# Kernel optimization log

Hardware: AMD Instinct MI355X
Metric: run time of the kernel (lower is better)

The kernel has to match this reference:

```python
import jax, jax.numpy as jnp
import numpy as np

N = 100000   # nodes
E = 1600000  # edges (before self-loops)
HIDDEN = 256
BN_EPS = 1e-5


def setup_inputs() -> dict:
    key = jax.random.key(0)
    ks = jax.random.split(key, 16)
    def lin(k, i, o):
        return jax.random.normal(k, (i, o), jnp.float32) / np.float32(np.sqrt(i))
    inp = {
        "x": jax.random.normal(ks[0], (N, 21), jnp.float32),
        "edge_index": jax.random.randint(ks[1], (2, E), 0, N),
        # GCNConv weights (stored [in, out]) + biases
        "W1": lin(ks[2], 21, HIDDEN), "b1": jnp.zeros((HIDDEN,), jnp.float32),
        "W2": lin(ks[3], HIDDEN, 112), "b2": jnp.zeros((112,), jnp.float32),
        # dense MLP
        "lin2_w": lin(ks[4], 112, 256), "lin2_b": jnp.zeros((256,), jnp.float32),
        "lin3_w": lin(ks[5], 256, 100), "lin3_b": jnp.zeros((100,), jnp.float32),
        "lin4_w": lin(ks[6], 100, 1),   "lin4_b": jnp.zeros((1,), jnp.float32),
        # batchnorm affine params
        "g1": jnp.ones((112,), jnp.float32), "be1": jnp.zeros((112,), jnp.float32),
        "g2": jnp.ones((256,), jnp.float32), "be2": jnp.zeros((256,), jnp.float32),
        "g3": jnp.ones((100,), jnp.float32), "be3": jnp.zeros((100,), jnp.float32),
    }
    return inp


def _gcn_conv(x, W, b, src, dst, n):
    # PyG GCNConv: h = xW; out_i = sum_j norm_ij * h_j (+ bias), sym-normalized w/ self-loops
    h = x @ W                                              # [N, C]
    deg = jax.ops.segment_sum(jnp.ones(src.shape, h.dtype), dst, num_segments=n)
    dinv = jnp.where(deg > 0, jax.lax.rsqrt(deg), 0.0)
    norm = dinv[src] * dinv[dst]                            # [E']
    out = jax.ops.segment_sum(h[src] * norm[:, None], dst, num_segments=n)
    return out + b


def _bn(x, g, b):
    # train-mode batchnorm: biased batch variance
    m = jnp.mean(x, axis=0)
    v = jnp.mean(jnp.square(x - m), axis=0)
    return (x - m) * jax.lax.rsqrt(v + BN_EPS) * g + b


def reference(x, edge_index, W1, b1, W2, b2, lin2_w, lin2_b, lin3_w, lin3_b,
              lin4_w, lin4_b, g1, be1, g2, be2, g3, be3):
    n = x.shape[0]
    loops = jnp.arange(n, dtype=edge_index.dtype)
    src = jnp.concatenate([edge_index[0], loops])
    dst = jnp.concatenate([edge_index[1], loops])
    h = jax.nn.relu(_gcn_conv(x, W1, b1, src, dst, n))
    h = _gcn_conv(h, W2, b2, src, dst, n)
    h = jax.nn.relu(_bn(h, g1, be1))
    # dropout: identity (eval / deterministic)
    h = jax.nn.relu(_bn(h @ lin2_w + lin2_b, g2, be2))
    h = jax.nn.relu(_bn(h @ lin3_w + lin3_b, g3, be3))
    return h @ lin4_w + lin4_b
```

## Files before the change

kernel.cpp:

```cpp
#include <hip/hip_runtime.h>

#define N_NODES 100000
#define N_EDGES 1600000

typedef _Float16 f16x8 __attribute__((ext_vector_type(8)));
typedef _Float16 f16x4 __attribute__((ext_vector_type(4)));
typedef float fx4 __attribute__((ext_vector_type(4)));

#define NREP 16
#define NBUCK 196
#define CHUNK 8192
#define BCAP 12288

__global__ __launch_bounds__(256) void k_bin(const int* __restrict__ ei,
                                             unsigned* __restrict__ binned,
                                             int* __restrict__ gcount) {
  __shared__ unsigned pr[CHUNK];
  __shared__ unsigned srt[CHUNK];
  __shared__ unsigned char bk[CHUNK];
  __shared__ int hist[256], scanb[256], offs[256], bs[256], gb[256];
  const int t = threadIdx.x;
  const int e0 = blockIdx.x * CHUNK;
  const int n = min(CHUNK, N_EDGES - e0);
  hist[t] = 0;
  __syncthreads();
  for (int i = t; i < n; i += 256) {
    int src = ei[e0 + i], dst = ei[N_EDGES + e0 + i];
    int b = dst >> 9;
    pr[i] = ((unsigned)src << 9) | (unsigned)(dst & 511);
    bk[i] = (unsigned char)b;
    atomicAdd(&hist[b], 1);
  }
  __syncthreads();
  int v = hist[t];
  scanb[t] = v;
  __syncthreads();
  for (int off = 1; off < 256; off <<= 1) {
    int a = (t >= off) ? scanb[t - off] : 0;
    __syncthreads();
    scanb[t] += a;
    __syncthreads();
  }
  offs[t] = scanb[t] - v;
  bs[t] = scanb[t] - v;
  __syncthreads();
  for (int i = t; i < n; i += 256) {
    int b = bk[i];
    int p = atomicAdd(&offs[b], 1);
    srt[p] = pr[i];
  }
  if (t < NBUCK && v > 0) gb[t] = atomicAdd(&gcount[t], v);
  __syncthreads();
  int wave = t >> 6, lane = t & 63;
  for (int b = wave; b < NBUCK; b += 4) {
    int c = hist[b];
    if (c == 0) continue;
    int ls = bs[b], base = gb[b];
    unsigned* dstp = binned + (size_t)b * BCAP + base;
    for (int i = lane; i < c; i += 64) dstp[i] = srt[ls + i];
  }
}

__global__ void k_bscan(const int* __restrict__ gcount, int* __restrict__ gbase) {
  __shared__ int s[256];
  int t = threadIdx.x;
  int v = (t < NBUCK) ? gcount[t] : 0;
  s[t] = v;
  __syncthreads();
  for (int off = 1; off < 256; off <<= 1) {
    int a = (t >= off) ? s[t - off] : 0;
    __syncthreads();
    s[t] += a;
    __syncthreads();
  }
  if (t < NBUCK) gbase[t] = s[t] - v;
}

__global__ __launch_bounds__(256) void k_csr(const unsigned* __restrict__ binned,
                                             const int* __restrict__ gcount,
                                             const int* __restrict__ gbase,
                                             int* __restrict__ rowoff,
                                             int* __restrict__ cnt,
                                             float* __restrict__ dinv,
                                             int* __restrict__ csr) {
  __shared__ int hist[512], offs[512], ps[256];
  __shared__ unsigned srt[BCAP];
  const int b = blockIdx.x, t = threadIdx.x;
  const int n = min(gcount[b], BCAP);
  const int gb0 = gbase[b];
  const unsigned* bp = binned + (size_t)b * BCAP;
  hist[t] = 0;
  hist[t + 256] = 0;
  __syncthreads();
  for (int i = t; i < n; i += 256) atomicAdd(&hist[bp[i] & 511], 1);
  __syncthreads();
  int e0v = hist[2 * t], e1v = hist[2 * t + 1];
  ps[t] = e0v + e1v;
  __syncthreads();
  for (int off = 1; off < 256; off <<= 1) {
    int a = (t >= off) ? ps[t - off] : 0;
    __syncthreads();
    ps[t] += a;
    __syncthreads();
  }
  int excl = ps[t] - (e0v + e1v);
  offs[2 * t] = excl;
  offs[2 * t + 1] = excl + e0v;
  __syncthreads();
#pragma unroll
  for (int u = 0; u < 2; ++u) {
    int j = 2 * t + u;
    int nd = (b << 9) + j;
    if (nd < N_NODES) {
      int c = hist[j];
      cnt[nd] = c;
      dinv[nd] = rsqrtf((float)(c + 1));
      rowoff[nd] = gb0 + offs[j];
    }
  }
  __syncthreads();
  for (int i = t; i < n; i += 256) {
    unsigned p = bp[i];
    int d = p & 511;
    int pos = atomicAdd(&offs[d], 1);
    srt[pos] = p >> 9;
  }
  __syncthreads();
  for (int i = t; i < n; i += 256) csr[gb0 + i] = (int)srt[i];
}

__global__ void k_xpad(const float* __restrict__ x, const float* __restrict__ dinv,
                       _Float16* __restrict__ xs) {
  int idx = blockIdx.x * 256 + threadIdx.x;
  if (idx >= N_NODES * 24) return;
  int r = idx / 24, c = idx - r * 24;
  xs[idx] = (_Float16)((c < 21) ? x[r * 21 + c] * dinv[r] : 0.f);
}

__global__ __launch_bounds__(256) void k_aggx(
    const f16x8* __restrict__ xs3, const float* __restrict__ dinv,
    const int* __restrict__ rowoff, const int* __restrict__ cnt,
    const int* __restrict__ csr, float* __restrict__ aggx) {
  int lane = threadIdx.x & 63, wave = threadIdx.x >> 6;
  int j = lane / 3, c = lane - j * 3;
  if (j >= 21) return;
  int i = blockIdx.x * 84 + wave * 21 + j;
  if (i >= N_NODES) return;
  float di = dinv[i];
  int start = rowoff[i], len = cnt[i];
  f16x8 u = xs3[i * 3 + c];
  float a0[8], a1[8], a2[8], a3[8];
#pragma unroll
  for (int t = 0; t < 8; ++t) { a0[t] = (float)u[t]; a1[t] = a2[t] = a3[t] = 0.f; }
  int e = 0;
  for (; e + 3 < len; e += 4) {
    int s0 = csr[start + e], s1 = csr[start + e + 1];
    int s2 = csr[start + e + 2], s3 = csr[start + e + 3];
    f16x8 u0 = xs3[s0 * 3 + c];
    f16x8 u1 = xs3[s1 * 3 + c];
    f16x8 u2 = xs3[s2 * 3 + c];
    f16x8 u3 = xs3[s3 * 3 + c];
#pragma unroll
    for (int t = 0; t < 8; ++t) {
      a0[t] += (float)u0[t]; a1[t] += (float)u1[t];
      a2[t] += (float)u2[t]; a3[t] += (float)u3[t];
    }
  }
  for (; e < len; ++e) {
    int s0 = csr[start + e];
    f16x8 u0 = xs3[s0 * 3 + c];
#pragma unroll
    for (int t = 0; t < 8; ++t) a0[t] += (float)u0[t];
  }
  float4 r0, r1;
  r0.x = di * (a0[0] + a1[0] + a2[0] + a3[0]);
  r0.y = di * (a0[1] + a1[1] + a2[1] + a3[1]);
  r0.z = di * (a0[2] + a1[2] + a2[2] + a3[2]);
  r0.w = di * (a0[3] + a1[3] + a2[3] + a3[3]);
  r1.x = di * (a0[4] + a1[4] + a2[4] + a3[4]);
  r1.y = di * (a0[5] + a1[5] + a2[5] + a3[5]);
  r1.z = di * (a0[6] + a1[6] + a2[6] + a3[6]);
  r1.w = di * (a0[7] + a1[7] + a2[7] + a3[7]);
  *(float4*)(aggx + (size_t)i * 24 + c * 8) = r0;
  *(float4*)(aggx + (size_t)i * 24 + c * 8 + 4) = r1;
}

__global__ __launch_bounds__(256) void k_gemm1(const float4* __restrict__ aggx4,
                                               const float* __restrict__ W1,
                                               const float* __restrict__ b1,
                                               _Float16* __restrict__ h1) {
  __shared__ float As[32][24];
  int t = threadIdx.x;
  int base = blockIdx.x * 32;
  for (int idx = t; idx < 32 * 6; idx += 256) {
    int m = idx / 6, q = idx - m * 6;
    *(float4*)(&As[m][q * 4]) = aggx4[(base + m) * 6 + q];
  }
  float w[21];
#pragma unroll
  for (int k = 0; k < 21; ++k) w[k] = W1[k * 256 + t];
  float bias = b1[t];
  __syncthreads();
  for (int m = 0; m < 32; ++m) {
    float acc = bias;
#pragma unroll
    for (int k = 0; k < 21; ++k) acc = fmaf(As[m][k], w[k], acc);
    h1[(size_t)(base + m) * 256 + t] = (_Float16)fmaxf(acc, 0.f);
  }
}

template <int K, int KPAD, int NOUT, int NR>
__global__ void k_wcvt(const float* __restrict__ W, _Float16* __restrict__ Wh) {
  int idx = blockIdx.x * 256 + threadIdx.x;
  if (idx >= NR * KPAD) return;
  int n = idx / KPAD, k = idx % KPAD;
  float v = (n < NOUT && k < K) ? W[k * NOUT + n] : 0.f;
  Wh[idx] = (_Float16)v;
}

template <int K, int KPAD, int NT, int MT, int WR, int WC, int MINW,
          bool BN, bool STATS, bool F16OUT, bool SPLIT>
__global__ __launch_bounds__(256, MINW) void k_mgemm(
    const _Float16* __restrict__ A16, const _Float16* __restrict__ Wt,
    const float* __restrict__ bias, const float* __restrict__ bn_a,
    const float* __restrict__ bn_c, const float* __restrict__ rowscale,
    void* __restrict__ Cv, void* __restrict__ Cv2, int NOUTr,
    float* __restrict__ sums, float* __restrict__ sqs) {
  constexpr int BM = WR * MT * 16;
  constexpr int NR = WC * NT * 16;
  constexpr int BKP = 40;
  constexpr int NC = KPAD / 32;
  constexpr int AIT = BM * 4 / 256;
  constexpr int ABYTES = BM * BKP * 2;
  constexpr int BBYTES = NR * BKP * 2;
  __shared__ __align__(16) char smem[ABYTES + BBYTES];
  _Float16* Ah = (_Float16*)smem;
  _Float16* Bh = (_Float16*)(smem + ABYTES);
  float* C = (float*)Cv;
  _Float16* C16 = (_Float16*)Cv;
  _Float16* C16b = (_Float16*)Cv2;

  const int tid = threadIdx.x;
  const int lane = tid & 63, wave = tid >> 6;
  const int wr = wave % WR, wc = wave / WR;
  const int quad = lane >> 4, ln = lane & 15;
  const int rowbase = blockIdx.x * BM;

  fx4 acc[MT][NT];
#pragma unroll
  for (int mt = 0; mt < MT; ++mt)
#pragma unroll
    for (int j = 0; j < NT; ++j) acc[mt][j] = (fx4){0.f, 0.f, 0.f, 0.f};

  f16x8 pf16[AIT];

  auto loadA = [&](int kc) {
#pragma unroll
    for (int it = 0; it < AIT; ++it) {
      int idx = tid + it * 256;
      int m = idx >> 2, q = idx & 3;
      int gi = rowbase + m;
      int k = kc * 32 + q * 8;
      bool ok = (gi < N_NODES) && (k < K);
      f16x8 z;
#pragma unroll
      for (int t = 0; t < 8; ++t) z[t] = (_Float16)0;
      pf16[it] = ok ? *(const f16x8*)(A16 + (size_t)gi * K + k) : z;
    }
  };

  auto writeA = [&](int kc) {
#pragma unroll
    for (int it = 0; it < AIT; ++it) {
      int idx = tid + it * 256;
      int m = idx >> 2, q = idx & 3;
      int k = kc * 32 + q * 8;
      float vv[8];
#pragma unroll
      for (int t = 0; t < 8; ++t) vv[t] = (float)pf16[it][t];
      if constexpr (BN) {
        if (k < K) {
          float4 a0 = *(const float4*)(bn_a + k);
          float4 a1 = *(const float4*)(bn_a + k + 4);
          float4 c0 = *(const float4*)(bn_c + k);
          float4 c1 = *(const float4*)(bn_c + k + 4);
          float av[8] = {a0.x, a0.y, a0.z, a0.w, a1.x, a1.y, a1.z, a1.w};
          float cv[8] = {c0.x, c0.y, c0.z, c0.w, c1.x, c1.y, c1.z, c1.w};
#pragma unroll
          for (int t = 0; t < 8; ++t) vv[t] = fmaxf(fmaf(vv[t], av[t], cv[t]), 0.f);
        }
      }
      f16x8 hv;
#pragma unroll
      for (int t = 0; t < 8; ++t) hv[t] = (_Float16)vv[t];
      *(f16x8*)(Ah + m * BKP + q * 8) = hv;
    }
  };

  loadA(0);
  for (int kc = 0; kc < NC; ++kc) {
    __syncthreads();
    writeA(kc);
    for (int idx = tid; idx < NR * 4; idx += 256) {
      int n = idx >> 2, p = idx & 3;
      *(f16x8*)(Bh + n * BKP + p * 8) =
          *(const f16x8*)(Wt + n * KPAD + kc * 32 + p * 8);
    }
    __syncthreads();
    if (kc + 1 < NC) loadA(kc + 1);
    f16x8 nf[MT];
#pragma unroll
    for (int mt = 0; mt < MT; ++mt) {
      int r = (wr * MT + mt) * 16 + ln;
      nf[mt] = *(const f16x8*)(Ah + r * BKP + quad * 8);
    }
#pragma unroll
    for (int j = 0; j < NT; ++j) {
      int n = (wc * NT + j) * 16 + ln;
      f16x8 wh = *(const f16x8*)(Bh + n * BKP + quad * 8);
#pragma unroll
      for (int mt = 0; mt < MT; ++mt)
        acc[mt][j] = __builtin_amdgcn_mfma_f32_16x16x32_f16(wh, nf[mt], acc[mt][j], 0, 0, 0);
    }
  }

  float* s_s = (float*)smem;
  float* s_q = s_s + NR;
  __syncthreads();
  if constexpr (STATS) {
    for (int c = tid; c < 2 * NR; c += 256) s_s[c] = 0.f;
    __syncthreads();
  }
  float rs[MT];
#pragma unroll
  for (int mt = 0; mt < MT; ++mt) {
    int nd = rowbase + (wr * MT + mt) * 16 + ln;
    rs[mt] = (rowscale != nullptr && nd < N_NODES) ? rowscale[nd] : 1.f;
  }
#pragma unroll
  for (int j = 0; j < NT; ++j) {
    int ch0 = (wc * NT + j) * 16 + quad * 4;
    bool cv = ch0 < NOUTr;
    float4 b4 = make_float4(0.f, 0.f, 0.f, 0.f);
    if (cv && bias != nullptr) b4 = *(const float4*)(bias + ch0);
    float sc[4] = {0.f, 0.f, 0.f, 0.f}, sq[4] = {0.f, 0.f, 0.f, 0.f};
#pragma unroll
    for (int mt = 0; mt < MT; ++mt) {
      int nd = rowbase + (wr * MT + mt) * 16 + ln;
      if (nd < N_NODES && cv) {
        float v0 = (acc[mt][j][0] + b4.x) * rs[mt];
        float v1 = (acc[mt][j][1] + b4.y) * rs[mt];
        float v2 = (acc[mt][j][2] + b4.z) * rs[mt];
        float v3 = (acc[mt][j][3] + b4.w) * rs[mt];
        if constexpr (F16OUT) {
          f16x4 o = {(_Float16)v0, (_Float16)v1, (_Float16)v2, (_Float16)v3};
          if constexpr (SPLIT) {
            _Float16* dp = (ch0 < 56)
                ? C16 + (size_t)nd * 64 + ch0
                : C16b + (size_t)nd * 64 + (ch0 - 56);
            *(f16x4*)dp = o;
          } else {
            *(f16x4*)(C16 + (size_t)nd * NOUTr + ch0) = o;
          }
        } else {
          float4 o = make_float4(v0, v1, v2, v3);
          *(float4*)(C + (size_t)nd * NOUTr + ch0) = o;
        }
        if constexpr (STATS) {
          sc[0] += v0; sq[0] = fmaf(v0, v0, sq[0]);
          sc[1] += v1; sq[1] = fmaf(v1, v1, sq[1]);
          sc[2] += v2; sq[2] = fmaf(v2, v2, sq[2]);
          sc[3] += v3; sq[3] = fmaf(v3, v3, sq[3]);
        }
      }
    }
    if constexpr (STATS) {
      if (cv) {
#pragma unroll
        for (int r = 0; r < 4; ++r) {
          float s = sc[r], q = sq[r];
          s += __shfl_xor(s, 1); q += __shfl_xor(q, 1);
          s += __shfl_xor(s, 2); q += __shfl_xor(q, 2);
          s += __shfl_xor(s, 4); q += __shfl_xor(q, 4);
          s += __shfl_xor(s, 8); q += __shfl_xor(q, 8);
          if (ln == 0) {
            atomicAdd(&s_s[ch0 + r], s);
            atomicAdd(&s_q[ch0 + r], q);
          }
        }
      }
    }
  }
  if constexpr (STATS) {
    __syncthreads();
    int rep = (blockIdx.x & (NREP - 1));
    for (int c = tid; c < NR; c += 256) {
      if (c < NOUTr) {
        atomicAdd(&sums[rep * NOUTr + c], s_s[c]);
        atomicAdd(&sqs[rep * NOUTr + c], s_q[c]);
      }
    }
  }
}

template <int K, int KPAD, int NT, int MT, int MINW,
          bool BN, bool STATS, bool F16OUT>
__global__ __launch_bounds__(256, MINW) void k_mgemm2(
    const _Float16* __restrict__ A16, const _Float16* __restrict__ Wt,
    const float* __restrict__ bias, const float* __restrict__ bn_a,
    const float* __restrict__ bn_c, const float* __restrict__ rowscale,
    void* __restrict__ Cv, int NOUTr, float* __restrict__ sums,
    float* __restrict__ sqs) {
  constexpr int WR = 4;
  constexpr int BM = WR * MT * 16;
  constexpr int NR = NT * 16;
  constexpr int KPS = KPAD + 8;
  constexpr int NC = KPAD / 32;
  __shared__ __align__(16) _Float16 Bh[NR * KPS];

  const int tid = threadIdx.x;
  const int lane = tid & 63, wave = tid >> 6;
  const int quad = lane >> 4, ln = lane & 15;
  const int rowbase = blockIdx.x * BM;
  const int chbase = blockIdx.y * NR;

  for (int idx = tid; idx < NR * (KPAD / 8); idx += 256) {
    int n = idx / (KPAD / 8), p = idx % (KPAD / 8);
    *(f16x8*)(Bh + n * KPS + p * 8) =
        *(const f16x8*)(Wt + (size_t)(chbase + n) * KPAD + p * 8);
  }
  __syncthreads();

  fx4 acc[MT][NT];
#pragma unroll
  for (int mt = 0; mt < MT; ++mt)
#pragma unroll
    for (int j = 0; j < NT; ++j) acc[mt][j] = (fx4){0.f, 0.f, 0.f, 0.f};

  for (int kc = 0; kc < NC; ++kc) {
    const int k0 = kc * 32 + quad * 8;
    f16x8 af[MT];
#pragma unroll
    for (int mt = 0; mt < MT; ++mt) {
      int gi = rowbase + (wave * MT + mt) * 16 + ln;
      bool ok = (gi < N_NODES) && (k0 < K);
      f16x8 z;
#pragma unroll
      for (int t = 0; t < 8; ++t) z[t] = (_Float16)0;
      af[mt] = ok ? *(const f16x8*)(A16 + (size_t)gi * K + k0) : z;
    }
    if constexpr (BN) {
      if (k0 < K) {
        float4 ba0 = *(const float4*)(bn_a + k0);
        float4 ba1 = *(const float4*)(bn_a + k0 + 4);
        float4 bc0 = *(const float4*)(bn_c + k0);
        float4 bc1 = *(const float4*)(bn_c + k0 + 4);
        float av[8] = {ba0.x, ba0.y, ba0.z, ba0.w, ba1.x, ba1.y, ba1.z, ba1.w};
        float cv[8] = {bc0.x, bc0.y, bc0.z, bc0.w, bc1.x, bc1.y, bc1.z, bc1.w};
#pragma unroll
        for (int mt = 0; mt < MT; ++mt)
#pragma unroll
          for (int t = 0; t < 8; ++t)
            af[mt][t] = (_Float16)fmaxf(fmaf((float)af[mt][t], av[t], cv[t]), 0.f);
      }
    }
#pragma unroll
    for (int j = 0; j < NT; ++j) {
      f16x8 wh = *(const f16x8*)(Bh + (j * 16 + ln) * KPS + kc * 32 + quad * 8);
#pragma unroll
      for (int mt = 0; mt < MT; ++mt)
        acc[mt][j] = __builtin_amdgcn_mfma_f32_16x16x32_f16(wh, af[mt], acc[mt][j], 0, 0, 0);
    }
  }

  float* s_s = (float*)Bh;
  float* s_q = s_s + NR;
  __syncthreads();
  if constexpr (STATS) {
    for (int c = tid; c < 2 * NR; c += 256) s_s[c] = 0.f;
    __syncthreads();
  }
  float rs[MT];
#pragma unroll
  for (int mt = 0; mt < MT; ++mt) {
    int nd = rowbase + (wave * MT + mt) * 16 + ln;
    rs[mt] = (rowscale != nullptr && nd < N_NODES) ? rowscale[nd] : 1.f;
  }
  float* C = (float*)Cv;
  _Float16* C16 = (_Float16*)Cv;
#pragma unroll
  for (int j = 0; j < NT; ++j) {
    int lch = j * 16 + quad * 4;
    int ch0 = chbase + lch;
    bool cv = ch0 < NOUTr;
    float4 b4 = make_float4(0.f, 0.f, 0.f, 0.f);
    if (cv && bias != nullptr) b4 = *(const float4*)(bias + ch0);
    float sc[4] = {0.f, 0.f, 0.f, 0.f}, sq[4] = {0.f, 0.f, 0.f, 0.f};
#pragma unroll
    for (int mt = 0; mt < MT; ++mt) {
      int nd = rowbase + (wave * MT + mt) * 16 + ln;
      if (nd < N_NODES && cv) {
        float v0 = (acc[mt][j][0] + b4.x) * rs[mt];
        float v1 = (acc[mt][j][1] + b4.y) * rs[mt];
        float v2 = (acc[mt][j][2] + b4.z) * rs[mt];
        float v3 = (acc[mt][j][3] + b4.w) * rs[mt];
        if constexpr (F16OUT) {
          f16x4 o = {(_Float16)v0, (_Float16)v1, (_Float16)v2, (_Float16)v3};
          *(f16x4*)(C16 + (size_t)nd * NOUTr + ch0) = o;
        } else {
          float4 o = make_float4(v0, v1, v2, v3);
          *(float4*)(C + (size_t)nd * NOUTr + ch0) = o;
        }
        if constexpr (STATS) {
          sc[0] += v0; sq[0] = fmaf(v0, v0, sq[0]);
          sc[1] += v1; sq[1] = fmaf(v1, v1, sq[1]);
          sc[2] += v2; sq[2] = fmaf(v2, v2, sq[2]);
          sc[3] += v3; sq[3] = fmaf(v3, v3, sq[3]);
        }
      }
    }
    if constexpr (STATS) {
      if (cv) {
#pragma unroll
        for (int r = 0; r < 4; ++r) {
          float s = sc[r], q = sq[r];
          s += __shfl_xor(s, 1); q += __shfl_xor(q, 1);
          s += __shfl_xor(s, 2); q += __shfl_xor(q, 2);
          s += __shfl_xor(s, 4); q += __shfl_xor(q, 4);
          s += __shfl_xor(s, 8); q += __shfl_xor(q, 8);
          if (ln == 0) {
            atomicAdd(&s_s[lch + r], s);
            atomicAdd(&s_q[lch + r], q);
          }
        }
      }
    }
  }
  if constexpr (STATS) {
    __syncthreads();
    int rep = (blockIdx.x & (NREP - 1));
    for (int c = tid; c < NR; c += 256) {
      int gc = chbase + c;
      if (gc < NOUTr) {
        atomicAdd(&sums[rep * NOUTr + gc], s_s[c]);
        atomicAdd(&sqs[rep * NOUTr + gc], s_q[c]);
      }
    }
  }
}

__global__ __launch_bounds__(256) void k_agg2(
    const f16x8* __restrict__ t2x8, const float* __restrict__ dinv,
    const int* __restrict__ rowoff, const int* __restrict__ cnt,
    const int* __restrict__ csr, const float* __restrict__ b2,
    _Float16* __restrict__ g2, int off) {
  int lane = threadIdx.x & 63, wave = threadIdx.x >> 6;
  int j = lane >> 3, c = lane & 7;
  int i = blockIdx.x * 32 + wave * 8 + j;
  float di = dinv[i];
  int start = rowoff[i], len = cnt[i];
  f16x8 u = t2x8[i * 8 + c];
  float a0[8], a1[8], a2[8], a3[8];
#pragma unroll
  for (int t = 0; t < 8; ++t) { a0[t] = (float)u[t]; a1[t] = a2[t] = a3[t] = 0.f; }
  int e = 0;
  for (; e + 3 < len; e += 4) {
    int s0 = csr[start + e], s1 = csr[start + e + 1];
    int s2 = csr[start + e + 2], s3 = csr[start + e + 3];
    f16x8 u0 = t2x8[s0 * 8 + c];
    f16x8 u1 = t2x8[s1 * 8 + c];
    f16x8 u2 = t2x8[s2 * 8 + c];
    f16x8 u3 = t2x8[s3 * 8 + c];
#pragma unroll
    for (int t = 0; t < 8; ++t) {
      a0[t] += (float)u0[t]; a1[t] += (float)u1[t];
      a2[t] += (float)u2[t]; a3[t] += (float)u3[t];
    }
  }
  for (; e < len; ++e) {
    int s0 = csr[start + e];
    f16x8 u0 = t2x8[s0 * 8 + c];
#pragma unroll
    for (int t = 0; t < 8; ++t) a0[t] += (float)u0[t];
  }
  if (c < 7) {
    float4 blo = *(const float4*)(b2 + off + c * 8);
    float4 bhi = *(const float4*)(b2 + off + c * 8 + 4);
    float bb[8] = {blo.x, blo.y, blo.z, blo.w, bhi.x, bhi.y, bhi.z, bhi.w};
    f16x8 o;
#pragma unroll
    for (int t = 0; t < 8; ++t)
      o[t] = (_Float16)fmaf(di, a0[t] + a1[t] + a2[t] + a3[t], bb[t]);
    *(f16x8*)(g2 + (size_t)i * 112 + off + c * 8) = o;
  }
}

template <int C>
__global__ void k_colstats16(const _Float16* __restrict__ X, float* __restrict__ sums,
                             float* __restrict__ sqs) {
  int c = threadIdx.x;
  if (c >= C) return;
  int chunk = (N_NODES + gridDim.x - 1) / gridDim.x;
  int i0 = blockIdx.x * chunk;
  int i1 = min(N_NODES, i0 + chunk);
  float s = 0.f, q = 0.f;
  for (int i = i0; i < i1; ++i) {
    float v = (float)X[(size_t)i * C + c];
    s += v;
    q = fmaf(v, v, q);
  }
  int rep = (blockIdx.x & (NREP - 1));
  atomicAdd(&sums[rep * C + c], s);
  atomicAdd(&sqs[rep * C + c], q);
}

template <int C>
__global__ void k_bnfinal(const float* __restrict__ sums, const float* __restrict__ sqs,
                          const float* __restrict__ gamma, const float* __restrict__ beta,
                          float* __restrict__ bn_a, float* __restrict__ bn_c) {
  int c = threadIdx.x;
  if (c >= C) return;
  float s = 0.f, q = 0.f;
#pragma unroll
  for (int r = 0; r < NREP; ++r) {
    s += sums[r * C + c];
    q += sqs[r * C + c];
  }
  const float inv_n = 1.0f / (float)N_NODES;
  float mean = s * inv_n;
  float var = fmaxf(q * inv_n - mean * mean, 0.f);
  float rstd = 1.0f / sqrtf(var + 1e-5f);
  float a = gamma[c] * rstd;
  bn_a[c] = a;
  bn_c[c] = beta[c] - mean * a;
}

__global__ void k_final(const _Float16* __restrict__ h4, const float* __restrict__ bn_a,
                        const float* __restrict__ bn_c, const float* __restrict__ w4,
                        const float* __restrict__ b4, float* __restrict__ out) {
  int lane = threadIdx.x & 63;
  int i = blockIdx.x * 4 + (threadIdx.x >> 6);
  float acc = fmaxf(fmaf((float)h4[(size_t)i * 100 + lane], bn_a[lane], bn_c[lane]), 0.f) * w4[lane];
  if (lane < 36) {
    int k = lane + 64;
    acc += fmaxf(fmaf((float)h4[(size_t)i * 100 + k], bn_a[k], bn_c[k]), 0.f) * w4[k];
  }
#pragma unroll
  for (int off = 32; off >= 1; off >>= 1) acc += __shfl_down(acc, off);
  if (lane == 0) out[i] = acc + b4[0];
}

extern "C" void kernel_launch(void* const* d_in, const int* in_sizes, int n_in,
                              void* d_out, int out_size, void* d_ws, size_t ws_size,
                              hipStream_t stream) {
  const float* x   = (const float*)d_in[0];
  const int*   ei  = (const int*)d_in[1];
  const float* W1  = (const float*)d_in[2];
  const float* b1  = (const float*)d_in[3];
  const float* W2  = (const float*)d_in[4];
  const float* b2  = (const float*)d_in[5];
  const float* l2w = (const float*)d_in[6];
  const float* l2b = (const float*)d_in[7];
  const float* l3w = (const float*)d_in[8];
  const float* l3b = (const float*)d_in[9];
  const float* l4w = (const float*)d_in[10];
  const float* l4b = (const float*)d_in[11];
  const float* g1  = (const float*)d_in[12];
  const float* be1 = (const float*)d_in[13];
  const float* g2w = (const float*)d_in[14];
  const float* be2 = (const float*)d_in[15];
  const float* g3  = (const float*)d_in[16];
  const float* be3 = (const float*)d_in[17];
  float* out = (float*)d_out;

  char* base = (char*)d_ws;
  size_t off = 0;
  auto alloc = [&](size_t bytes) -> char* {
    char* p = base + off;
    off = (off + bytes + 255) & ~(size_t)255;
    return p;
  };
  int*   cnt    = (int*)alloc((size_t)N_NODES * 4);
  int*   rowoff = (int*)alloc((size_t)N_NODES * 4);
  float* dinv   = (float*)alloc((size_t)N_NODES * 4);
  int*   csr    = (int*)alloc((size_t)N_EDGES * 4);
  unsigned* binned = (unsigned*)alloc((size_t)NBUCK * BCAP * 4);
  int*   gcount = (int*)alloc(NBUCK * 4);
  int*   gbase  = (int*)alloc(NBUCK * 4);
  float* stats  = (float*)alloc((size_t)NREP * 960 * 4);
  float* bnco   = (float*)alloc(960 * 4);
  _Float16* xs  = (_Float16*)alloc((size_t)N_NODES * 24 * 2);
  float* aggx   = (float*)alloc((size_t)N_NODES * 24 * 4);
  _Float16* h1  = (_Float16*)alloc((size_t)N_NODES * 256 * 2);
  _Float16* t2a = (_Float16*)alloc((size_t)N_NODES * 64 * 2);
  _Float16* t2b = (_Float16*)alloc((size_t)N_NODES * 64 * 2);
  _Float16* g2h = (_Float16*)alloc((size_t)N_NODES * 112 * 2);
  _Float16* h4  = (_Float16*)alloc((size_t)N_NODES * 112 * 2);
  _Float16* wt2 = (_Float16*)alloc(112 * 256 * 2);
  _Float16* wt3 = (_Float16*)alloc(256 * 128 * 2);
  _Float16* wt4 = (_Float16*)alloc(112 * 256 * 2);

  float* sums1 = stats;
  float* sqs1  = sums1 + NREP * 112;
  float* sums2 = sqs1 + NREP * 112;
  float* sqs2  = sums2 + NREP * 256;
  float* sums3 = sqs2 + NREP * 256;
  float* sqs3  = sums3 + NREP * 112;
  float* bn_a1 = bnco + 0,   *bn_c1 = bnco + 112;
  float* bn_a2 = bnco + 224, *bn_c2 = bnco + 480;
  float* bn_a3 = bnco + 736, *bn_c3 = bnco + 848;

  hipMemsetAsync(gcount, 0, NBUCK * 4, stream);
  hipMemsetAsync(stats, 0, (size_t)NREP * 960 * 4, stream);

  k_bin<<<NBUCK, 256, 0, stream>>>(ei, binned, gcount);
  k_bscan<<<1, 256, 0, stream>>>(gcount, gbase);
  k_csr<<<NBUCK, 256, 0, stream>>>(binned, gcount, gbase, rowoff, cnt, dinv, csr);

  k_wcvt<256, 256, 112, 112><<<112, 256, 0, stream>>>(W2, wt2);
  k_wcvt<112, 128, 256, 256><<<128, 256, 0, stream>>>(l2w, wt3);
  k_wcvt<256, 256, 100, 112><<<112, 256, 0, stream>>>(l3w, wt4);

  k_xpad<<<(N_NODES * 24 + 255) / 256, 256, 0, stream>>>(x, dinv, xs);
  k_aggx<<<(N_NODES + 83) / 84, 256, 0, stream>>>((const f16x8*)xs, dinv, rowoff,
                                                  cnt, csr, aggx);
  k_gemm1<<<3125, 256, 0, stream>>>((const float4*)aggx, W1, b1, h1);

  k_mgemm<256, 256, 7, 2, 4, 1, 4, false, false, true, true>
      <<<782, 256, 0, stream>>>(h1, wt2, nullptr, nullptr, nullptr, dinv,
                                t2a, t2b, 112, nullptr, nullptr);
  k_agg2<<<3125, 256, 0, stream>>>((const f16x8*)t2a, dinv, rowoff, cnt, csr, b2,
                                   g2h, 0);
  k_agg2<<<3125, 256, 0, stream>>>((const f16x8*)t2b, dinv, rowoff, cnt, csr, b2,
                                   g2h, 56);

  k_colstats16<112><<<1600, 128, 0, stream>>>(g2h, sums1, sqs1);
  k_bnfinal<112><<<1, 128, 0, stream>>>(sums1, sqs1, g1, be1, bn_a1, bn_c1);

  k_mgemm2<112, 128, 8, 2, 3, true, true, true>
      <<<dim3(782, 2), 256, 0, stream>>>(g2h, wt3, l2b, bn_a1, bn_c1, nullptr,
                                         h1, 256, sums2, sqs2);
  k_bnfinal<256><<<1, 256, 0, stream>>>(sums2, sqs2, g2w, be2, bn_a2, bn_c2);

  k_mgemm<256, 256, 7, 2, 4, 1, 4, true, true, true, false>
      <<<782, 256, 0, stream>>>(h1, wt4, l3b, bn_a2, bn_c2, nullptr,
                                h4, nullptr, 100, sums3, sqs3);
  k_bnfinal<100><<<1, 128, 0, stream>>>(sums3, sqs3, g3, be3, bn_a3, bn_c3);

  k_final<<<25000, 256, 0, stream>>>(h4, bn_a3, bn_c3, l4w, l4b, out);
}
```

Measured before the change: 410.6 us.

## Fuse bucket scan, x padding, weight converts and BN1 stats into neighbor kernels

Result: slower. 430.7 us (+4.9%).

```diff
diff --git a/kernel.cpp b/kernel.cpp
--- a/kernel.cpp
+++ b/kernel.cpp
@@ -61,37 +61,36 @@
   }
 }
 
-__global__ void k_bscan(const int* __restrict__ gcount, int* __restrict__ gbase) {
-  __shared__ int s[256];
-  int t = threadIdx.x;
-  int v = (t < NBUCK) ? gcount[t] : 0;
-  s[t] = v;
-  __syncthreads();
-  for (int off = 1; off < 256; off <<= 1) {
-    int a = (t >= off) ? s[t - off] : 0;
-    __syncthreads();
-    s[t] += a;
-    __syncthreads();
-  }
-  if (t < NBUCK) gbase[t] = s[t] - v;
-}
-
 __global__ __launch_bounds__(256) void k_csr(const unsigned* __restrict__ binned,
                                              const int* __restrict__ gcount,
-                                             const int* __restrict__ gbase,
                                              int* __restrict__ rowoff,
                                              int* __restrict__ cnt,
                                              float* __restrict__ dinv,
-                                             int* __restrict__ csr) {
-  __shared__ int hist[512], offs[512], ps[256];
+                                             int* __restrict__ csr,
+                                             const float* __restrict__ x,
+                                             _Float16* __restrict__ xs) {
+  __shared__ int hist[512], offs[512], ps[256], gsc[256];
+  __shared__ int sh_gb0;
   __shared__ unsigned srt[BCAP];
   const int b = blockIdx.x, t = threadIdx.x;
-  const int n = min(gcount[b], BCAP);
-  const int gb0 = gbase[b];
   const unsigned* bp = binned + (size_t)b * BCAP;
+
+  int vb = (t < NBUCK) ? gcount[t] : 0;
+  gsc[t] = vb;
+  __syncthreads();
+  for (int off = 1; off < 256; off <<= 1) {
+    int a = (t >= off) ? gsc[t - off] : 0;
+    __syncthreads();
+    gsc[t] += a;
+    __syncthreads();
+  }
+  if (t == b) sh_gb0 = gsc[t] - vb;
   hist[t] = 0;
   hist[t + 256] = 0;
   __syncthreads();
+  const int gb0 = sh_gb0;
+  const int n = min(gcount[b], BCAP);
+
   for (int i = t; i < n; i += 256) atomicAdd(&hist[bp[i] & 511], 1);
   __syncthreads();
   int e0v = hist[2 * t], e1v = hist[2 * t + 1];
@@ -118,6 +117,14 @@
       rowoff[nd] = gb0 + offs[j];
     }
   }
+  for (int idx = t; idx < 512 * 24; idx += 256) {
+    int j = idx / 24, c = idx - j * 24;
+    int nd = (b << 9) + j;
+    if (nd < N_NODES) {
+      float dv = rsqrtf((float)(hist[j] + 1));
+      xs[(size_t)nd * 24 + c] = (_Float16)((c < 21) ? x[(size_t)nd * 21 + c] * dv : 0.f);
+    }
+  }
   __syncthreads();
   for (int i = t; i < n; i += 256) {
     unsigned p = bp[i];
@@ -127,14 +134,6 @@
   }
   __syncthreads();
   for (int i = t; i < n; i += 256) csr[gb0 + i] = (int)srt[i];
-}
-
-__global__ void k_xpad(const float* __restrict__ x, const float* __restrict__ dinv,
-                       _Float16* __restrict__ xs) {
-  int idx = blockIdx.x * 256 + threadIdx.x;
-  if (idx >= N_NODES * 24) return;
-  int r = idx / 24, c = idx - r * 24;
-  xs[idx] = (_Float16)((c < 21) ? x[r * 21 + c] * dinv[r] : 0.f);
 }
 
 __global__ __launch_bounds__(256) void k_aggx(
@@ -209,13 +208,23 @@
   }
 }
 
-template <int K, int KPAD, int NOUT, int NR>
-__global__ void k_wcvt(const float* __restrict__ W, _Float16* __restrict__ Wh) {
+__global__ void k_wcvt_all(const float* __restrict__ W2, const float* __restrict__ l2w,
+                           const float* __restrict__ l3w, _Float16* __restrict__ wt2,
+                           _Float16* __restrict__ wt3, _Float16* __restrict__ wt4) {
   int idx = blockIdx.x * 256 + threadIdx.x;
-  if (idx >= NR * KPAD) return;
-  int n = idx / KPAD, k = idx % KPAD;
-  float v = (n < NOUT && k < K) ? W[k * NOUT + n] : 0.f;
-  Wh[idx] = (_Float16)v;
+  const int S1 = 112 * 256, S2 = 256 * 128, S3 = 112 * 256;
+  if (idx < S1) {
+    int n = idx / 256, k = idx % 256;
+    wt2[idx] = (_Float16)W2[k * 112 + n];
+  } else if (idx < S1 + S2) {
+    int r = idx - S1;
+    int n = r / 128, k = r % 128;
+    wt3[r] = (_Float16)((k < 112) ? l2w[k * 256 + n] : 0.f);
+  } else if (idx < S1 + S2 + S3) {
+    int r = idx - S1 - S2;
+    int n = r / 256, k = r % 256;
+    wt4[r] = (_Float16)((n < 100) ? l3w[k * 100 + n] : 0.f);
+  }
 }
 
 template <int K, int KPAD, int NT, int MT, int WR, int WC, int MINW,
@@ -553,10 +562,14 @@
     const f16x8* __restrict__ t2x8, const float* __restrict__ dinv,
     const int* __restrict__ rowoff, const int* __restrict__ cnt,
     const int* __restrict__ csr, const float* __restrict__ b2,
-    _Float16* __restrict__ g2, int off) {
-  int lane = threadIdx.x & 63, wave = threadIdx.x >> 6;
+    _Float16* __restrict__ g2, int off, float* __restrict__ sums,
+    float* __restrict__ sqs) {
+  __shared__ float s_s[56], s_q[56];
+  int tid = threadIdx.x;
+  int lane = tid & 63, wave = tid >> 6;
   int j = lane >> 3, c = lane & 7;
   int i = blockIdx.x * 32 + wave * 8 + j;
+  if (tid < 56) { s_s[tid] = 0.f; s_q[tid] = 0.f; }
   float di = dinv[i];
   int start = rowoff[i], len = cnt[i];
   f16x8 u = t2x8[i * 8 + c];
@@ -583,35 +596,38 @@
 #pragma unroll
     for (int t = 0; t < 8; ++t) a0[t] += (float)u0[t];
   }
-  if (c < 7) {
+  float ov[8];
+  {
     float4 blo = *(const float4*)(b2 + off + c * 8);
     float4 bhi = *(const float4*)(b2 + off + c * 8 + 4);
     float bb[8] = {blo.x, blo.y, blo.z, blo.w, bhi.x, bhi.y, bhi.z, bhi.w};
     f16x8 o;
 #pragma unroll
-    for (int t = 0; t < 8; ++t)
-      o[t] = (_Float16)fmaf(di, a0[t] + a1[t] + a2[t] + a3[t], bb[t]);
-    *(f16x8*)(g2 + (size_t)i * 112 + off + c * 8) = o;
-  }
-}
-
-template <int C>
-__global__ void k_colstats16(const _Float16* __restrict__ X, float* __restrict__ sums,
-                             float* __restrict__ sqs) {
-  int c = threadIdx.x;
-  if (c >= C) return;
-  int chunk = (N_NODES + gridDim.x - 1) / gridDim.x;
-  int i0 = blockIdx.x * chunk;
-  int i1 = min(N_NODES, i0 + chunk);
-  float s = 0.f, q = 0.f;
-  for (int i = i0; i < i1; ++i) {
-    float v = (float)X[(size_t)i * C + c];
-    s += v;
-    q = fmaf(v, v, q);
-  }
+    for (int t = 0; t < 8; ++t) {
+      ov[t] = fmaf(di, a0[t] + a1[t] + a2[t] + a3[t], bb[t]);
+      o[t] = (_Float16)ov[t];
+    }
+    if (c < 7) *(f16x8*)(g2 + (size_t)i * 112 + off + c * 8) = o;
+  }
+  __syncthreads();
+#pragma unroll
+  for (int t = 0; t < 8; ++t) {
+    float s = (c < 7) ? ov[t] : 0.f;
+    float q = (c < 7) ? ov[t] * ov[t] : 0.f;
+    s += __shfl_xor(s, 8);  q += __shfl_xor(q, 8);
+    s += __shfl_xor(s, 16); q += __shfl_xor(q, 16);
+    s += __shfl_xor(s, 32); q += __shfl_xor(q, 32);
+    if (j == 0 && c < 7) {
+      atomicAdd(&s_s[c * 8 + t], s);
+      atomicAdd(&s_q[c * 8 + t], q);
+    }
+  }
+  __syncthreads();
   int rep = (blockIdx.x & (NREP - 1));
-  atomicAdd(&sums[rep * C + c], s);
-  atomicAdd(&sqs[rep * C + c], q);
+  if (tid < 56) {
+    atomicAdd(&sums[rep * 112 + off + tid], s_s[tid]);
+    atomicAdd(&sqs[rep * 112 + off + tid], s_q[tid]);
+  }
 }
 
 template <int C>
@@ -686,7 +702,6 @@
   int*   csr    = (int*)alloc((size_t)N_EDGES * 4);
   unsigned* binned = (unsigned*)alloc((size_t)NBUCK * BCAP * 4);
   int*   gcount = (int*)alloc(NBUCK * 4);
-  int*   gbase  = (int*)alloc(NBUCK * 4);
   float* stats  = (float*)alloc((size_t)NREP * 960 * 4);
   float* bnco   = (float*)alloc(960 * 4);
   _Float16* xs  = (_Float16*)alloc((size_t)N_NODES * 24 * 2);
@@ -714,14 +729,10 @@
   hipMemsetAsync(stats, 0, (size_t)NREP * 960 * 4, stream);
 
   k_bin<<<NBUCK, 256, 0, stream>>>(ei, binned, gcount);
-  k_bscan<<<1, 256, 0, stream>>>(gcount, gbase);
-  k_csr<<<NBUCK, 256, 0, stream>>>(binned, gcount, gbase, rowoff, cnt, dinv, csr);
-
-  k_wcvt<256, 256, 112, 112><<<112, 256, 0, stream>>>(W2, wt2);
-  k_wcvt<112, 128, 256, 256><<<128, 256, 0, stream>>>(l2w, wt3);
-  k_wcvt<256, 256, 100, 112><<<112, 256, 0, stream>>>(l3w, wt4);
-
-  k_xpad<<<(N_NODES * 24 + 255) / 256, 256, 0, stream>>>(x, dinv, xs);
+  k_csr<<<NBUCK, 256, 0, stream>>>(binned, gcount, rowoff, cnt, dinv, csr, x, xs);
+
+  k_wcvt_all<<<352, 256, 0, stream>>>(W2, l2w, l3w, wt2, wt3, wt4);
+
   k_aggx<<<(N_NODES + 83) / 84, 256, 0, stream>>>((const f16x8*)xs, dinv, rowoff,
                                                   cnt, csr, aggx);
   k_gemm1<<<3125, 256, 0, stream>>>((const float4*)aggx, W1, b1, h1);
@@ -730,11 +741,9 @@
       <<<782, 256, 0, stream>>>(h1, wt2, nullptr, nullptr, nullptr, dinv,
                                 t2a, t2b, 112, nullptr, nullptr);
   k_agg2<<<3125, 256, 0, stream>>>((const f16x8*)t2a, dinv, rowoff, cnt, csr, b2,
-                                   g2h, 0);
+                                   g2h, 0, sums1, sqs1);
   k_agg2<<<3125, 256, 0, stream>>>((const f16x8*)t2b, dinv, rowoff, cnt, csr, b2,
-                                   g2h, 56);
-
-  k_colstats16<112><<<1600, 128, 0, stream>>>(g2h, sums1, sqs1);
+                                   g2h, 56, sums1, sqs1);
   k_bnfinal<112><<<1, 128, 0, stream>>>(sums1, sqs1, g1, be1, bn_a1, bn_c1);
 
   k_mgemm2<112, 128, 8, 2, 3, true, true, true>
```
